# Performance work log

Measured on AMD Instinct MI355X. Metric: run time of the kernel, lower is better.

Reference implementation:

```python
import jax, jax.numpy as jnp
import numpy as np

NUM_GRAPHS = 1024

def setup_inputs() -> dict:
    key = jax.random.key(0)
    ks = jax.random.split(key, 6)
    N, E = 500000, 16000000
    x = jax.random.normal(ks[0], (N, 4), dtype=jnp.float32)
    edge_index = jax.random.randint(ks[1], (2, E), 0, N, dtype=jnp.int32)
    batch = jnp.sort(jax.random.randint(ks[2], (N,), 0, NUM_GRAPHS, dtype=jnp.int32))
    eps = jnp.zeros((), dtype=jnp.float32)
    W1 = jax.random.normal(ks[3], (4, 16), dtype=jnp.float32) * 0.5
    b1 = jnp.zeros((16,), dtype=jnp.float32)
    W2 = jax.random.normal(ks[4], (16, 4), dtype=jnp.float32) * 0.25
    b2 = jnp.zeros((4,), dtype=jnp.float32)
    return {"x": x, "edge_index": edge_index, "batch": batch,
            "eps": eps, "W1": W1, "b1": b1, "W2": W2, "b2": b2}

def reference(x, edge_index, batch, eps, W1, b1, W2, b2):
    N = x.shape[0]
    src, dst = edge_index[0], edge_index[1]
    # GINConv aggregation: sum of neighbor (source) features at each target node
    agg = jax.ops.segment_sum(x[src], dst, num_segments=N)  # [N, 4]
    h = (1.0 + eps) * x + agg
    # 2-layer MLP: Lin(4,16) -> ReLU -> Lin(16,4)
    h = jax.nn.relu(h @ W1 + b1) @ W2 + b2
    h = jax.nn.relu(h)
    # global_mean_pool over batch segment ids
    sums = jax.ops.segment_sum(h, batch, num_segments=NUM_GRAPHS)      # [G, 4]
    cnts = jax.ops.segment_sum(jnp.ones((N,), h.dtype), batch, num_segments=NUM_GRAPHS)
    pooled = sums / jnp.maximum(cnts, 1.0)[:, None]
    return jax.nn.log_softmax(pooled, axis=1)
```

## Files before the change

kernel.cpp:

```cpp
#include <hip/hip_runtime.h>

#define NUM_GRAPHS 1024
#define BIN_BITS 10
#define BIN_SIZE (1 << BIN_BITS)
#define EB 4096
#define STH 512
#define EPT 8
#define SWAVES 8
#define CURS 16
#define ACCTH 256
#define ACCW 4

typedef int v4i __attribute__((ext_vector_type(4)));

__device__ inline unsigned bf16_rn(float f) {
    unsigned u = __float_as_uint(f);
    return (u + 0x7FFFu + ((u >> 16) & 1u)) >> 16;
}

__global__ void __launch_bounds__(STH, 6) bin_scatter(const float4* __restrict__ x,
                                                      uint2* __restrict__ x16,
                                                      const int* __restrict__ src,
                                                      const int* __restrict__ dst,
                                                      int* __restrict__ packed,
                                                      int* __restrict__ cursor,
                                                      int N, int E, int cap, int nb) {
    __shared__ int hist[SWAVES][512];
    __shared__ int wbase[SWAVES][512];

    const int t = threadIdx.x;
    const int lane = t & 63;
    const int wave = t >> 6;
    const int b0 = blockIdx.x * EB;
    const int myBase = b0 + t * EPT;

    {
        int nd = blockIdx.x * STH + t;
        if (nd < N) {
            float4 v = x[nd];
            uint2 r;
            r.x = bf16_rn(v.x) | (bf16_rn(v.y) << 16);
            r.y = bf16_rn(v.z) | (bf16_rn(v.w) << 16);
            x16[nd] = r;
        }
    }

    for (int j = t; j < SWAVES * 512; j += STH) (&hist[0][0])[j] = 0;
    __syncthreads();

    int dbuf[EPT], sbuf[EPT];
    const bool full = (myBase + EPT <= E);
    if (full) {
        *(int4*)(dbuf)     = *(const int4*)(dst + myBase);
        *(int4*)(dbuf + 4) = *(const int4*)(dst + myBase + 4);
        *(int4*)(sbuf)     = *(const int4*)(src + myBase);
        *(int4*)(sbuf + 4) = *(const int4*)(src + myBase + 4);
    } else {
#pragma unroll
        for (int i = 0; i < EPT; ++i) {
            int e = myBase + i;
            bool ok = e < E;
            dbuf[i] = ok ? dst[e] : 0;
            sbuf[i] = ok ? src[e] : 0;
        }
    }

    int pv[EPT];
    int bnlp[EPT];
#pragma unroll
    for (int k = 0; k < EPT; ++k) {
        int e = myBase + k;
        bool ok = full || (e < E);
        int d = dbuf[k];
        int bn = ((unsigned)d) >> BIN_BITS;
        pv[k] = ((d & (BIN_SIZE - 1)) << 19) | sbuf[k];
        unsigned long long m = __ballot(ok);
#pragma unroll
        for (int bb = 0; bb < 9; ++bb) {
            unsigned long long bm = __ballot((bn >> bb) & 1);
            m &= ((bn >> bb) & 1) ? bm : ~bm;
        }
        int rank = (int)__popcll(m & ((1ull << lane) - 1ull));
        int cnt  = (int)__popcll(m);
        int leader = __ffsll((unsigned long long)m) - 1;
        int old = hist[wave][bn];
        if (ok && lane == leader) hist[wave][bn] = old + cnt;
        bnlp[k] = ok ? ((bn << 16) | (old + rank)) : -1;
    }
    __syncthreads();

    {
        int c[SWAVES];
        int total = 0;
#pragma unroll
        for (int w = 0; w < SWAVES; ++w) { c[w] = hist[w][t]; total += c[w]; }
        int base = t * cap;
        if (t < nb && total > 0) base += atomicAdd(&cursor[t * CURS], total);
        int acc = base;
#pragma unroll
        for (int w = 0; w < SWAVES; ++w) { wbase[w][t] = acc; acc += c[w]; }
    }
    __syncthreads();

    if (full) {
#pragma unroll
        for (int k = 0; k < EPT; ++k) {
            int bn = ((unsigned)bnlp[k]) >> 16;
            int lp = bnlp[k] & 0xFFFF;
            int pos = wbase[wave][bn] + lp;
            if (pos < (bn + 1) * cap)
                packed[pos] = pv[k];
        }
    } else {
#pragma unroll
        for (int k = 0; k < EPT; ++k) {
            if (bnlp[k] >= 0) {
                int bn = ((unsigned)bnlp[k]) >> 16;
                int lp = bnlp[k] & 0xFFFF;
                int pos = wbase[wave][bn] + lp;
                if (pos < (bn + 1) * cap)
                    packed[pos] = pv[k];
            }
        }
    }
}

#define LOADR(B, PE, VM) do {                                              \
    int _i = (B) + lane * 4;                                               \
    if (_i + 3 < s1) {                                                     \
        v4i _p4 = __builtin_nontemporal_load((const v4i*)(packed + _i));   \
        PE[0] = _p4.x; PE[1] = _p4.y; PE[2] = _p4.z; PE[3] = _p4.w;        \
        VM = 0xF;                                                          \
    } else {                                                               \
        VM = 0;                                                            \
        PE[0] = (_i + 0 < s1) ? (VM |= 1, packed[_i + 0]) : 0;             \
        PE[1] = (_i + 1 < s1) ? (VM |= 2, packed[_i + 1]) : 0;             \
        PE[2] = (_i + 2 < s1) ? (VM |= 4, packed[_i + 2]) : 0;             \
        PE[3] = (_i + 3 < s1) ? (VM |= 8, packed[_i + 3]) : 0;             \
    }                                                                      \
} while (0)

#define GATHR(PE, G) do {                                                  \
    G[0] = x16[PE[0] & 0x7FFFF];                                           \
    G[1] = x16[PE[1] & 0x7FFFF];                                           \
    G[2] = x16[PE[2] & 0x7FFFF];                                           \
    G[3] = x16[PE[3] & 0x7FFFF];                                           \
} while (0)

#define PROCR(PE, G, VM) do {                                              \
    _Pragma("unroll")                                                      \
    for (int k = 0; k < 4; ++k) {                                          \
        int p = PE[k];                                                     \
        int dl = (((unsigned)p) >> 19) & (BIN_SIZE - 1);                   \
        unsigned long long m = ~0ull;                                      \
        _Pragma("unroll")                                                  \
        for (int bb = 0; bb < BIN_BITS; ++bb) {                            \
            unsigned long long bm = __ballot((dl >> bb) & 1);              \
            m &= ((dl >> bb) & 1) ? bm : ~bm;                              \
        }                                                                  \
        int rank = (int)__popcll(m & ((1ull << lane) - 1ull));             \
        float sc = ((VM >> k) & 1) ? 1.0f : 0.0f;                          \
        float v0 = __uint_as_float(G[k].x << 16) * sc;                     \
        float v1 = __uint_as_float(G[k].x & 0xFFFF0000u) * sc;             \
        float v2 = __uint_as_float(G[k].y << 16) * sc;                     \
        float v3 = __uint_as_float(G[k].y & 0xFFFF0000u) * sc;             \
                      \
        unsigned long long rem =                                           \
            (rank == 0) ? (m & ~(1ull << lane)) : 0ull;                    \
        while (__any(rem != 0)) {                                          \
            int srcl = rem ? (__ffsll((unsigned long long)rem) - 1) : 0;   \
            float t0 = __shfl(v0, srcl);                                   \
            float t1 = __shfl(v1, srcl);                                   \
            float t2 = __shfl(v2, srcl);                                   \
            float t3 = __shfl(v3, srcl);                                   \
            if (rem) { v0 += t0; v1 += t1; v2 += t2; v3 += t3;             \
                       rem &= rem - 1; }                                   \
        }                                                                  \
        if (rank == 0) {                                                   \
            float4* pp = (float4*)&planes[wave][dl][0];                    \
            float4 a = *pp;                                                \
            a.x += v0; a.y += v1; a.z += v2; a.w += v3;                    \
            *pp = a;                                                       \
        }                                                                  \
    }                                                                      \
} while (0)

__global__ void __launch_bounds__(ACCTH) bin_accum_mlp_pool(
        const float4* __restrict__ x,
        const uint2* __restrict__ x16,
        const int* __restrict__ packed,
        const int* __restrict__ cursor,
        const int* __restrict__ batch,
        const float* __restrict__ eps_p,
        const float* __restrict__ W1, const float* __restrict__ b1,
        const float* __restrict__ W2, const float* __restrict__ b2,
        float* __restrict__ gsum, float* __restrict__ gcnt,
        int N, int cap) {
    __shared__ float planes[ACCW][BIN_SIZE][4];

    const int bin = blockIdx.x;
    const int t = threadIdx.x;
    const int lane = t & 63;
    const int wave = t >> 6;

    {
        float4* pz = (float4*)&planes[0][0][0];
        float4 z; z.x = 0.f; z.y = 0.f; z.z = 0.f; z.w = 0.f;
#pragma unroll
        for (int i = 0; i < 16; ++i) pz[t + i * ACCTH] = z;
    }
    __syncthreads();

    const int start = bin * cap;
    int cnt = cursor[bin * CURS];
    if (cnt > cap) cnt = cap;
    if (cnt < 0) cnt = 0;
    const int end = start + cnt;

    int seg = ((cnt + ACCW - 1) / ACCW + 3) & ~3;
    int s0 = start + wave * seg;
    int s1 = s0 + seg; if (s1 > end) s1 = end;

    if (s0 < s1) {
        int peA[4], peB[4], vmA, vmB;
        uint2 gA[4], gB[4];
        int b = s0;
        LOADR(b, peA, vmA);
        GATHR(peA, gA);
        for (;;) {
            int b1n = b + 256;
            if (b1n < s1) { LOADR(b1n, peB, vmB); GATHR(peB, gB); }
            PROCR(peA, gA, vmA);
            if (b1n >= s1) break;
            int b2n = b1n + 256;
            if (b2n < s1) { LOADR(b2n, peA, vmA); GATHR(peA, gA); }
            PROCR(peB, gB, vmB);
            if (b2n >= s1) break;
            b = b2n;
        }
    }
    __syncthreads();

    const float eps = eps_p[0];
    for (int half = 0; half < 4; ++half) {
        int node = t + half * ACCTH;
        float4 a = *(const float4*)&planes[0][node][0];
#pragma unroll
        for (int w = 1; w < ACCW; ++w) {
            float4 bq = *(const float4*)&planes[w][node][0];
            a.x += bq.x; a.y += bq.y; a.z += bq.z; a.w += bq.w;
        }

        int n = bin * BIN_SIZE + node;
        bool valid = n < N;
        float o0 = 0.f, o1 = 0.f, o2 = 0.f, o3 = 0.f;
        int g = -1;
        if (valid) {
            float4 xv = x[n];
            float h0 = (1.0f + eps) * xv.x + a.x;
            float h1 = (1.0f + eps) * xv.y + a.y;
            float h2 = (1.0f + eps) * xv.z + a.z;
            float h3 = (1.0f + eps) * xv.w + a.w;

            float tmp[16];
#pragma unroll
            for (int j = 0; j < 16; ++j) {
                float v = b1[j] + h0 * W1[j] + h1 * W1[16 + j] + h2 * W1[32 + j] + h3 * W1[48 + j];
                tmp[j] = v > 0.0f ? v : 0.0f;
            }
            float o[4];
#pragma unroll
            for (int j = 0; j < 4; ++j) {
                float v = b2[j];
#pragma unroll
                for (int k = 0; k < 16; ++k) v += tmp[k] * W2[k * 4 + j];
                o[j] = v > 0.0f ? v : 0.0f;
            }
            o0 = o[0]; o1 = o[1]; o2 = o[2]; o3 = o[3];
            g = batch[n];
        }

        int g0 = __shfl(g, 0);
        bool uni = __all(g == g0);
        if (uni && g0 >= 0) {
#pragma unroll
            for (int off = 32; off > 0; off >>= 1) {
                o0 += __shfl_down(o0, off);
                o1 += __shfl_down(o1, off);
                o2 += __shfl_down(o2, off);
                o3 += __shfl_down(o3, off);
            }
            if (lane == 0) {
                unsafeAtomicAdd(&gsum[(size_t)g0 * 4 + 0], o0);
                unsafeAtomicAdd(&gsum[(size_t)g0 * 4 + 1], o1);
                unsafeAtomicAdd(&gsum[(size_t)g0 * 4 + 2], o2);
                unsafeAtomicAdd(&gsum[(size_t)g0 * 4 + 3], o3);
                unsafeAtomicAdd(&gcnt[g0], 64.0f);
            }
        } else if (valid) {
            unsafeAtomicAdd(&gsum[(size_t)g * 4 + 0], o0);
            unsafeAtomicAdd(&gsum[(size_t)g * 4 + 1], o1);
            unsafeAtomicAdd(&gsum[(size_t)g * 4 + 2], o2);
            unsafeAtomicAdd(&gsum[(size_t)g * 4 + 3], o3);
            unsafeAtomicAdd(&gcnt[g], 1.0f);
        }
    }
}

__global__ void pool_softmax_kernel(const float* __restrict__ gsum,
                                    const float* __restrict__ gcnt,
                                    float* __restrict__ out) {
    int g = blockIdx.x * blockDim.x + threadIdx.x;
    if (g >= NUM_GRAPHS) return;
    float c = fmaxf(gcnt[g], 1.0f);
    float p0 = gsum[g * 4 + 0] / c;
    float p1 = gsum[g * 4 + 1] / c;
    float p2 = gsum[g * 4 + 2] / c;
    float p3 = gsum[g * 4 + 3] / c;
    float m = fmaxf(fmaxf(p0, p1), fmaxf(p2, p3));
    float s = expf(p0 - m) + expf(p1 - m) + expf(p2 - m) + expf(p3 - m);
    float lse = m + logf(s);
    out[g * 4 + 0] = p0 - lse;
    out[g * 4 + 1] = p1 - lse;
    out[g * 4 + 2] = p2 - lse;
    out[g * 4 + 3] = p3 - lse;
}

__global__ void edge_scatter_kernel(const float4* __restrict__ x,
                                    const int* __restrict__ src,
                                    const int* __restrict__ dst,
                                    float* __restrict__ agg,
                                    int E) {
    int t = blockIdx.x * blockDim.x + threadIdx.x;
    int e = t * 4;
    if (e + 3 < E) {
        int4 s = *(const int4*)(src + e);
        int4 d = *(const int4*)(dst + e);
        float4 xv;
        xv = x[s.x];
        unsafeAtomicAdd(&agg[(size_t)d.x * 4 + 0], xv.x);
        unsafeAtomicAdd(&agg[(size_t)d.x * 4 + 1], xv.y);
        unsafeAtomicAdd(&agg[(size_t)d.x * 4 + 2], xv.z);
        unsafeAtomicAdd(&agg[(size_t)d.x * 4 + 3], xv.w);
        xv = x[s.y];
        unsafeAtomicAdd(&agg[(size_t)d.y * 4 + 0], xv.x);
        unsafeAtomicAdd(&agg[(size_t)d.y * 4 + 1], xv.y);
        unsafeAtomicAdd(&agg[(size_t)d.y * 4 + 2], xv.z);
        unsafeAtomicAdd(&agg[(size_t)d.y * 4 + 3], xv.w);
        xv = x[s.z];
        unsafeAtomicAdd(&agg[(size_t)d.z * 4 + 0], xv.x);
        unsafeAtomicAdd(&agg[(size_t)d.z * 4 + 1], xv.y);
        unsafeAtomicAdd(&agg[(size_t)d.z * 4 + 2], xv.z);
        unsafeAtomicAdd(&agg[(size_t)d.z * 4 + 3], xv.w);
        xv = x[s.w];
        unsafeAtomicAdd(&agg[(size_t)d.w * 4 + 0], xv.x);
        unsafeAtomicAdd(&agg[(size_t)d.w * 4 + 1], xv.y);
        unsafeAtomicAdd(&agg[(size_t)d.w * 4 + 2], xv.z);
        unsafeAtomicAdd(&agg[(size_t)d.w * 4 + 3], xv.w);
    } else {
        for (int i = e; i < E; ++i) {
            int sv = src[i], dv = dst[i];
            float4 xv = x[sv];
            unsafeAtomicAdd(&agg[(size_t)dv * 4 + 0], xv.x);
            unsafeAtomicAdd(&agg[(size_t)dv * 4 + 1], xv.y);
            unsafeAtomicAdd(&agg[(size_t)dv * 4 + 2], xv.z);
            unsafeAtomicAdd(&agg[(size_t)dv * 4 + 3], xv.w);
        }
    }
}

__global__ void node_mlp_pool_kernel(const float4* __restrict__ x,
                                     const float4* __restrict__ agg,
                                     const int* __restrict__ batch,
                                     const float* __restrict__ eps_p,
                                     const float* __restrict__ W1,
                                     const float* __restrict__ b1,
                                     const float* __restrict__ W2,
                                     const float* __restrict__ b2,
                                     float* __restrict__ gsum,
                                     float* __restrict__ gcnt,
                                     int N) {
    int i = blockIdx.x * blockDim.x + threadIdx.x;
    bool valid = i < N;
    float o0 = 0.f, o1 = 0.f, o2 = 0.f, o3 = 0.f;
    int g = -1;
    if (valid) {
        float eps = eps_p[0];
        float4 xv = x[i];
        float4 av = agg[i];
        float h0 = (1.0f + eps) * xv.x + av.x;
        float h1 = (1.0f + eps) * xv.y + av.y;
        float h2 = (1.0f + eps) * xv.z + av.z;
        float h3 = (1.0f + eps) * xv.w + av.w;
        float tmp[16];
#pragma unroll
        for (int j = 0; j < 16; ++j) {
            float v = b1[j] + h0 * W1[j] + h1 * W1[16 + j] + h2 * W1[32 + j] + h3 * W1[48 + j];
            tmp[j] = v > 0.0f ? v : 0.0f;
        }
        float o[4];
#pragma unroll
        for (int j = 0; j < 4; ++j) {
            float v = b2[j];
#pragma unroll
            for (int k = 0; k < 16; ++k) v += tmp[k] * W2[k * 4 + j];
            o[j] = v > 0.0f ? v : 0.0f;
        }
        o0 = o[0]; o1 = o[1]; o2 = o[2]; o3 = o[3];
        g = batch[i];
    }
    int g0 = __shfl(g, 0);
    bool uni = __all(g == g0);
    if (uni && g0 >= 0) {
#pragma unroll
        for (int off = 32; off > 0; off >>= 1) {
            o0 += __shfl_down(o0, off);
            o1 += __shfl_down(o1, off);
            o2 += __shfl_down(o2, off);
            o3 += __shfl_down(o3, off);
        }
        if ((threadIdx.x & 63) == 0) {
            unsafeAtomicAdd(&gsum[(size_t)g0 * 4 + 0], o0);
            unsafeAtomicAdd(&gsum[(size_t)g0 * 4 + 1], o1);
            unsafeAtomicAdd(&gsum[(size_t)g0 * 4 + 2], o2);
            unsafeAtomicAdd(&gsum[(size_t)g0 * 4 + 3], o3);
            unsafeAtomicAdd(&gcnt[g0], 64.0f);
        }
    } else if (valid) {
        unsafeAtomicAdd(&gsum[(size_t)g * 4 + 0], o0);
        unsafeAtomicAdd(&gsum[(size_t)g * 4 + 1], o1);
        unsafeAtomicAdd(&gsum[(size_t)g * 4 + 2], o2);
        unsafeAtomicAdd(&gsum[(size_t)g * 4 + 3], o3);
        unsafeAtomicAdd(&gcnt[g], 1.0f);
    }
}

extern "C" void kernel_launch(void* const* d_in, const int* in_sizes, int n_in,
                              void* d_out, int out_size, void* d_ws, size_t ws_size,
                              hipStream_t stream) {
    const float* x     = (const float*)d_in[0];
    const int*   ei    = (const int*)d_in[1];
    const int*   batch = (const int*)d_in[2];
    const float* eps   = (const float*)d_in[3];
    const float* W1    = (const float*)d_in[4];
    const float* b1    = (const float*)d_in[5];
    const float* W2    = (const float*)d_in[6];
    const float* b2    = (const float*)d_in[7];

    const int N = in_sizes[0] / 4;
    const int E = in_sizes[1] / 2;
    const int* src = ei;
    const int* dst = ei + (size_t)E;

    const int nb = (N + BIN_SIZE - 1) >> BIN_BITS;
    const int epb = (E + nb - 1) / nb;
    int cap = epb + epb / 8 + 1024;
    cap = (cap + 3) & ~3;

    size_t x16_elems = ((size_t)2 * N + 3) & ~(size_t)3;
    size_t packed_elems = ((size_t)nb * cap + 3) & ~(size_t)3;
    size_t need = (x16_elems + packed_elems + 512 * CURS + NUM_GRAPHS * 5) * sizeof(float);

    int nblocks_e = (E + EB - 1) / EB;
    bool prep_ok = (size_t)nblocks_e * STH >= (size_t)N;

    if (nb <= 512 && N < (1 << 19) && need <= ws_size && prep_ok) {
        uint2* x16    = (uint2*)d_ws;
        int*   packed = (int*)d_ws + x16_elems;
        int*   cursor = packed + packed_elems;
        float* gsum   = (float*)(cursor + 512 * CURS);
        float* gcnt   = gsum + (size_t)NUM_GRAPHS * 4;

        (void)hipMemsetAsync(cursor, 0,
                             (512 * CURS + NUM_GRAPHS * 5) * sizeof(int), stream);

        bin_scatter<<<nblocks_e, STH, 0, stream>>>(
            (const float4*)x, x16, src, dst, packed, cursor, N, E, cap, nb);

        bin_accum_mlp_pool<<<nb, ACCTH, 0, stream>>>(
            (const float4*)x, (const uint2*)x16, packed, cursor, batch, eps,
            W1, b1, W2, b2, gsum, gcnt, N, cap);

        pool_softmax_kernel<<<(NUM_GRAPHS + 255) / 256, 256, 0, stream>>>(
            gsum, gcnt, (float*)d_out);
    } else {
        float* agg  = (float*)d_ws;
        float* gsum = agg + (size_t)N * 4;
        float* gcnt = gsum + (size_t)NUM_GRAPHS * 4;
        size_t zero_bytes = ((size_t)N * 4 + NUM_GRAPHS * 5) * sizeof(float);
        (void)hipMemsetAsync(d_ws, 0, zero_bytes, stream);

        int e4 = (E + 3) / 4;
        edge_scatter_kernel<<<(e4 + 255) / 256, 256, 0, stream>>>(
            (const float4*)x, src, dst, agg, E);

        node_mlp_pool_kernel<<<(N + 255) / 256, 256, 0, stream>>>(
            (const float4*)x, (const float4*)agg, batch, eps, W1, b1, W2, b2,
            gsum, gcnt, N);

        pool_softmax_kernel<<<(NUM_GRAPHS + 255) / 256, 256, 0, stream>>>(
            gsum, gcnt, (float*)d_out);
    }
}
```

Baseline: 429.6 us.

## Split each bin across two blocks with bf16 LDS planes and global atomic merge

After: 585.8 us. 1.36x slower.

```diff
diff --git a/kernel.cpp b/kernel.cpp
--- a/kernel.cpp
+++ b/kernel.cpp
@@ -10,6 +10,7 @@
 #define CURS 16
 #define ACCTH 256
 #define ACCW 4
+#define SPLIT 2
 
 typedef int v4i __attribute__((ext_vector_type(4)));
 
@@ -164,23 +165,18 @@
         float v1 = __uint_as_float(G[k].x & 0xFFFF0000u) * sc;             \
         float v2 = __uint_as_float(G[k].y << 16) * sc;                     \
         float v3 = __uint_as_float(G[k].y & 0xFFFF0000u) * sc;             \
-                      \
-        unsigned long long rem =                                           \
-            (rank == 0) ? (m & ~(1ull << lane)) : 0ull;                    \
-        while (__any(rem != 0)) {                                          \
-            int srcl = rem ? (__ffsll((unsigned long long)rem) - 1) : 0;   \
-            float t0 = __shfl(v0, srcl);                                   \
-            float t1 = __shfl(v1, srcl);                                   \
-            float t2 = __shfl(v2, srcl);                                   \
-            float t3 = __shfl(v3, srcl);                                   \
-            if (rem) { v0 += t0; v1 += t1; v2 += t2; v3 += t3;             \
-                       rem &= rem - 1; }                                   \
-        }                                                                  \
-        if (rank == 0) {                                                   \
-            float4* pp = (float4*)&planes[wave][dl][0];                    \
-            float4 a = *pp;                                                \
-            a.x += v0; a.y += v1; a.z += v2; a.w += v3;                    \
-            *pp = a;                                                       \
+        uint2* pp = &pl[wave][dl];                                         \
+        for (int pass = 0; __any(rank >= pass); ++pass) {                  \
+            if (rank == pass) {                                            \
+                uint2 c = *pp;                                             \
+                float c0 = __uint_as_float(c.x << 16) + v0;                \
+                float c1 = __uint_as_float(c.x & 0xFFFF0000u) + v1;        \
+                float c2 = __uint_as_float(c.y << 16) + v2;                \
+                float c3 = __uint_as_float(c.y & 0xFFFF0000u) + v3;        \
+                c.x = bf16_rn(c0) | (bf16_rn(c1) << 16);                   \
+                c.y = bf16_rn(c2) | (bf16_rn(c3) << 16);                   \
+                *pp = c;                                                   \
+            }                                                              \
         }                                                                  \
     }                                                                      \
 } while (0)
@@ -195,19 +191,21 @@
         const float* __restrict__ W1, const float* __restrict__ b1,
         const float* __restrict__ W2, const float* __restrict__ b2,
         float* __restrict__ gsum, float* __restrict__ gcnt,
+        float* __restrict__ agg, int* __restrict__ done,
         int N, int cap) {
-    __shared__ float planes[ACCW][BIN_SIZE][4];
-
-    const int bin = blockIdx.x;
+    __shared__ uint2 pl[ACCW][BIN_SIZE];
+    __shared__ int tick;
+
+    const int bin = blockIdx.x >> 1;
+    const int sp  = blockIdx.x & 1;
     const int t = threadIdx.x;
     const int lane = t & 63;
     const int wave = t >> 6;
 
     {
-        float4* pz = (float4*)&planes[0][0][0];
-        float4 z; z.x = 0.f; z.y = 0.f; z.z = 0.f; z.w = 0.f;
-#pragma unroll
-        for (int i = 0; i < 16; ++i) pz[t + i * ACCTH] = z;
+        uint2 z; z.x = 0u; z.y = 0u;
+#pragma unroll
+        for (int i = 0; i < 16; ++i) (&pl[0][0])[t + i * ACCTH] = z;
     }
     __syncthreads();
 
@@ -215,41 +213,53 @@
     int cnt = cursor[bin * CURS];
     if (cnt > cap) cnt = cap;
     if (cnt < 0) cnt = 0;
-    const int end = start + cnt;
-
-    int seg = ((cnt + ACCW - 1) / ACCW + 3) & ~3;
-    int s0 = start + wave * seg;
-    int s1 = s0 + seg; if (s1 > end) s1 = end;
-
-    if (s0 < s1) {
-        int peA[4], peB[4], vmA, vmB;
-        uint2 gA[4], gB[4];
-        int b = s0;
-        LOADR(b, peA, vmA);
-        GATHR(peA, gA);
-        for (;;) {
-            int b1n = b + 256;
-            if (b1n < s1) { LOADR(b1n, peB, vmB); GATHR(peB, gB); }
-            PROCR(peA, gA, vmA);
-            if (b1n >= s1) break;
-            int b2n = b1n + 256;
-            if (b2n < s1) { LOADR(b2n, peA, vmA); GATHR(peA, gA); }
-            PROCR(peB, gB, vmB);
-            if (b2n >= s1) break;
-            b = b2n;
-        }
+
+    int half = ((cnt + SPLIT - 1) / SPLIT + 3) & ~3;
+    int h0 = start + sp * half;
+    int h1 = h0 + half; if (h1 > start + cnt) h1 = start + cnt;
+    int hcnt = h1 - h0; if (hcnt < 0) hcnt = 0;
+    int wseg = ((hcnt + ACCW - 1) / ACCW + 3) & ~3;
+    int s0 = h0 + wave * wseg;
+    int s1 = s0 + wseg; if (s1 > h1) s1 = h1;
+
+    for (int b = s0; b < s1; b += 256) {
+        int pe[4]; int vm; uint2 g[4];
+        LOADR(b, pe, vm);
+        GATHR(pe, g);
+        PROCR(pe, g, vm);
     }
     __syncthreads();
 
+    float* aggb = agg + (size_t)bin * (BIN_SIZE * 4);
+#pragma unroll
+    for (int i = 0; i < 4; ++i) {
+        int node = t + i * ACCTH;
+        float r0 = 0.f, r1 = 0.f, r2 = 0.f, r3 = 0.f;
+#pragma unroll
+        for (int w = 0; w < ACCW; ++w) {
+            uint2 c = pl[w][node];
+            r0 += __uint_as_float(c.x << 16);
+            r1 += __uint_as_float(c.x & 0xFFFF0000u);
+            r2 += __uint_as_float(c.y << 16);
+            r3 += __uint_as_float(c.y & 0xFFFF0000u);
+        }
+        unsafeAtomicAdd(&aggb[node * 4 + 0], r0);
+        unsafeAtomicAdd(&aggb[node * 4 + 1], r1);
+        unsafeAtomicAdd(&aggb[node * 4 + 2], r2);
+        unsafeAtomicAdd(&aggb[node * 4 + 3], r3);
+    }
+    __threadfence();
+    if (t == 0) tick = atomicAdd(&done[bin], 1);
+    __syncthreads();
+    if (tick != SPLIT - 1) return;
+
     const float eps = eps_p[0];
-    for (int half = 0; half < 4; ++half) {
-        int node = t + half * ACCTH;
-        float4 a = *(const float4*)&planes[0][node][0];
-#pragma unroll
-        for (int w = 1; w < ACCW; ++w) {
-            float4 bq = *(const float4*)&planes[w][node][0];
-            a.x += bq.x; a.y += bq.y; a.z += bq.z; a.w += bq.w;
-        }
+    for (int hb = 0; hb < 4; ++hb) {
+        int node = t + hb * ACCTH;
+        float a0 = unsafeAtomicAdd(&aggb[node * 4 + 0], 0.0f);
+        float a1 = unsafeAtomicAdd(&aggb[node * 4 + 1], 0.0f);
+        float a2 = unsafeAtomicAdd(&aggb[node * 4 + 2], 0.0f);
+        float a3 = unsafeAtomicAdd(&aggb[node * 4 + 3], 0.0f);
 
         int n = bin * BIN_SIZE + node;
         bool valid = n < N;
@@ -257,15 +267,15 @@
         int g = -1;
         if (valid) {
             float4 xv = x[n];
-            float h0 = (1.0f + eps) * xv.x + a.x;
-            float h1 = (1.0f + eps) * xv.y + a.y;
-            float h2 = (1.0f + eps) * xv.z + a.z;
-            float h3 = (1.0f + eps) * xv.w + a.w;
+            float h0f = (1.0f + eps) * xv.x + a0;
+            float h1f = (1.0f + eps) * xv.y + a1;
+            float h2f = (1.0f + eps) * xv.z + a2;
+            float h3f = (1.0f + eps) * xv.w + a3;
 
             float tmp[16];
 #pragma unroll
             for (int j = 0; j < 16; ++j) {
-                float v = b1[j] + h0 * W1[j] + h1 * W1[16 + j] + h2 * W1[32 + j] + h3 * W1[48 + j];
+                float v = b1[j] + h0f * W1[j] + h1f * W1[16 + j] + h2f * W1[32 + j] + h3f * W1[48 + j];
                 tmp[j] = v > 0.0f ? v : 0.0f;
             }
             float o[4];
@@ -459,7 +469,8 @@
 
     size_t x16_elems = ((size_t)2 * N + 3) & ~(size_t)3;
     size_t packed_elems = ((size_t)nb * cap + 3) & ~(size_t)3;
-    size_t need = (x16_elems + packed_elems + 512 * CURS + NUM_GRAPHS * 5) * sizeof(float);
+    size_t zero_elems = 512 * CURS + 512 + NUM_GRAPHS * 5 + (size_t)512 * 4096;
+    size_t need = (x16_elems + packed_elems + zero_elems) * sizeof(float);
 
     int nblocks_e = (E + EB - 1) / EB;
     bool prep_ok = (size_t)nblocks_e * STH >= (size_t)N;
@@ -468,18 +479,19 @@
         uint2* x16    = (uint2*)d_ws;
         int*   packed = (int*)d_ws + x16_elems;
         int*   cursor = packed + packed_elems;
-        float* gsum   = (float*)(cursor + 512 * CURS);
+        int*   done   = cursor + 512 * CURS;
+        float* gsum   = (float*)(done + 512);
         float* gcnt   = gsum + (size_t)NUM_GRAPHS * 4;
-
-        (void)hipMemsetAsync(cursor, 0,
-                             (512 * CURS + NUM_GRAPHS * 5) * sizeof(int), stream);
+        float* agg    = gcnt + NUM_GRAPHS;
+
+        (void)hipMemsetAsync(cursor, 0, zero_elems * sizeof(int), stream);
 
         bin_scatter<<<nblocks_e, STH, 0, stream>>>(
             (const float4*)x, x16, src, dst, packed, cursor, N, E, cap, nb);
 
-        bin_accum_mlp_pool<<<nb, ACCTH, 0, stream>>>(
+        bin_accum_mlp_pool<<<nb * SPLIT, ACCTH, 0, stream>>>(
             (const float4*)x, (const uint2*)x16, packed, cursor, batch, eps,
-            W1, b1, W2, b2, gsum, gcnt, N, cap);
+            W1, b1, W2, b2, gsum, gcnt, agg, done, N, cap);
 
         pool_softmax_kernel<<<(NUM_GRAPHS + 255) / 256, 256, 0, stream>>>(
             gsum, gcnt, (float*)d_out);
```
